# Kernel tuning notes

Hardware: AMD Instinct MI355X
Metric: run time of the kernel (lower is better)

## Reference

```python
import jax, jax.numpy as jnp
import numpy as np

SEQ, B = 1, 250  # fixed by module's hardcoded reshapes


def gru_scan(x_seq, h0, Wih, Whh, bih, bhh):
    """PyTorch-convention GRU. x_seq: (S,B,In), h0: (B,H). Returns (y (S,B,H), hN (B,H))."""
    H = h0.shape[-1]

    def step(h, x_t):
        gi = x_t @ Wih.T + bih            # (B, 3H)
        gh = h @ Whh.T + bhh              # (B, 3H)
        i_r, i_z, i_n = jnp.split(gi, 3, axis=-1)
        h_r, h_z, h_n = jnp.split(gh, 3, axis=-1)
        r = jax.nn.sigmoid(i_r + h_r)
        z = jax.nn.sigmoid(i_z + h_z)
        n = jnp.tanh(i_n + r * h_n)
        h_new = (1.0 - z) * n + z * h
        return h_new, h_new

    hN, y = jax.lax.scan(step, h0, x_seq)
    return y, hN


def setup_inputs() -> dict:
    key = jax.random.key(0)
    ks = jax.random.split(key, 13)
    s = 0.1
    return {
        "x": jax.random.normal(ks[0], (250,), dtype=jnp.float32),
        "enc_Wih": jax.random.normal(ks[1], (12, 1), dtype=jnp.float32) * s,
        "enc_Whh": jax.random.normal(ks[2], (12, 4), dtype=jnp.float32) * s,
        "enc_bih": jax.random.normal(ks[3], (12,), dtype=jnp.float32) * s,
        "enc_bhh": jax.random.normal(ks[4], (12,), dtype=jnp.float32) * s,
        "fc1_W": jax.random.normal(ks[5], (512, 1000), dtype=jnp.float32) * 0.03,
        "fc1_b": jax.random.normal(ks[6], (512,), dtype=jnp.float32) * s,
        "fc2_W": jax.random.normal(ks[7], (250, 512), dtype=jnp.float32) * 0.04,
        "fc2_b": jax.random.normal(ks[8], (250,), dtype=jnp.float32) * s,
        "dec_Wih": jax.random.normal(ks[9], (3, 4), dtype=jnp.float32) * s,
        "dec_Whh": jax.random.normal(ks[10], (3, 1), dtype=jnp.float32) * s,
        "dec_bih": jax.random.normal(ks[11], (3,), dtype=jnp.float32) * s,
        "dec_bhh": jax.random.normal(ks[12], (3,), dtype=jnp.float32) * s,
    }


def reference(x, enc_Wih, enc_Whh, enc_bih, enc_bhh, fc1_W, fc1_b, fc2_W, fc2_b,
              dec_Wih, dec_Whh, dec_bih, dec_bhh):
    # Encoder
    x_seq = x.reshape(SEQ, B, 1)                      # (1, 250, 1)
    h0_enc = jnp.zeros((B, 4), dtype=x.dtype)
    y, hN = gru_scan(x_seq, h0_enc, enc_Wih, enc_Whh, enc_bih, enc_bhh)  # y (1,250,4)
    stacked = hN.reshape(1, 1000)
    hn_hid = jax.nn.relu(stacked @ fc1_W.T + fc1_b)   # (1, 512)
    hn = hn_hid @ fc2_W.T + fc2_b                     # (1, 250)
    # Decoder
    h0_dec = hn.reshape(B, 1)                         # (250, 1)
    yrec, _ = gru_scan(y, h0_dec, dec_Wih, dec_Whh, dec_bih, dec_bhh)    # (1, 250, 1)
    return yrec.reshape(250, 1)
```

## Files before the change

kernel.cpp:

```cpp
#include <hip/hip_runtime.h>
#include <math.h>

__device__ __forceinline__ float sigm(float x) { return 1.0f / (1.0f + __expf(-x)); }

__device__ __forceinline__ void enc_step(float xb, const float* __restrict__ Wih,
                                         const float* __restrict__ bih,
                                         const float* __restrict__ bhh, float h[4]) {
#pragma unroll
    for (int j = 0; j < 4; ++j) {
        float ir = fmaf(xb, Wih[j],     bih[j])     + bhh[j];
        float iz = fmaf(xb, Wih[4 + j], bih[4 + j]) + bhh[4 + j];
        float in_ = fmaf(xb, Wih[8 + j], bih[8 + j]);
        float hn  = bhh[8 + j];
        float r = sigm(ir);
        float z = sigm(iz);
        float n = tanhf(fmaf(r, hn, in_));
        h[j] = (1.0f - z) * n;
    }
}

__global__ __launch_bounds__(256) void fused(const float* __restrict__ x,
                                             const float* __restrict__ eWih,
                                             const float* __restrict__ ebih,
                                             const float* __restrict__ ebhh,
                                             const float* __restrict__ fc1W,
                                             const float* __restrict__ fc1b,
                                             const float* __restrict__ fc2W,
                                             const float* __restrict__ fc2b,
                                             const float* __restrict__ dWih,
                                             const float* __restrict__ dWhh,
                                             const float* __restrict__ dbih,
                                             const float* __restrict__ dbhh,
                                             float* __restrict__ partial,
                                             unsigned* __restrict__ counter,
                                             float* __restrict__ out) {
    __shared__ float stacked[1000];
    __shared__ float hid4[4];
    __shared__ unsigned oldc;
    const int t = threadIdx.x;
    const int wave = t >> 6, lane = t & 63;
    const int b = blockIdx.x;

    if (t < 250) {
        float h[4];
        enc_step(x[t], eWih, ebih, ebhh, h);
        ((float4*)stacked)[t] = make_float4(h[0], h[1], h[2], h[3]);
    }
    __syncthreads();

    const int j = b * 4 + wave;
    const float4* w4 = (const float4*)(fc1W + j * 1000);
    const float4* s4 = (const float4*)stacked;
    float s = 0.0f;
#pragma unroll
    for (int q = 0; q < 4; ++q) {
        const int k = lane + q * 64;
        if (k < 250) {
            float4 a = s4[k], w = w4[k];
            s = fmaf(a.x, w.x, s);
            s = fmaf(a.y, w.y, s);
            s = fmaf(a.z, w.z, s);
            s = fmaf(a.w, w.w, s);
        }
    }
#pragma unroll
    for (int m = 32; m >= 1; m >>= 1) s += __shfl_xor(s, m, 64);
    if (lane == 0) hid4[wave] = fmaxf(s + fc1b[j], 0.0f);
    __syncthreads();

    const float h0 = hid4[0], h1 = hid4[1], h2 = hid4[2], h3 = hid4[3];
    if (t < 250) {
        const float4 w2 = *(const float4*)(fc2W + t * 512 + b * 4);
        float p = fmaf(w2.x, h0, fmaf(w2.y, h1, fmaf(w2.z, h2, w2.w * h3)));
        __hip_atomic_store(&partial[b * 256 + t], p,
                           __ATOMIC_RELAXED, __HIP_MEMORY_SCOPE_AGENT);
    }
    asm volatile("s_waitcnt vmcnt(0)" ::: "memory");
    __syncthreads();

    if (t == 0)
        oldc = __hip_atomic_fetch_add(counter, 1u,
                                      __ATOMIC_RELAXED, __HIP_MEMORY_SCOPE_AGENT);
    __syncthreads();
    if ((oldc & 127u) != 127u) return;

    if (t < 250) {
        float acc = fc2b[t];
#pragma unroll 32
        for (int bb = 0; bb < 128; ++bb) {
            const float p = __hip_atomic_load(&partial[bb * 256 + t],
                                              __ATOMIC_RELAXED, __HIP_MEMORY_SCOPE_AGENT);
            acc += p;
        }
        const float hn_i = acc;

        const float y0 = stacked[t * 4 + 0], y1 = stacked[t * 4 + 1];
        const float y2 = stacked[t * 4 + 2], y3 = stacked[t * 4 + 3];
        float gi[3];
#pragma unroll
        for (int g = 0; g < 3; ++g) {
            gi[g] = fmaf(y0, dWih[g * 4 + 0],
                    fmaf(y1, dWih[g * 4 + 1],
                    fmaf(y2, dWih[g * 4 + 2],
                    fmaf(y3, dWih[g * 4 + 3], dbih[g]))));
        }
        const float gh0 = fmaf(hn_i, dWhh[0], dbhh[0]);
        const float gh1 = fmaf(hn_i, dWhh[1], dbhh[1]);
        const float gh2 = fmaf(hn_i, dWhh[2], dbhh[2]);
        const float r = sigm(gi[0] + gh0);
        const float z = sigm(gi[1] + gh1);
        const float n = tanhf(fmaf(r, gh2, gi[2]));
        out[t] = fmaf(z, hn_i, (1.0f - z) * n);
    }
}

extern "C" void kernel_launch(void* const* d_in, const int* in_sizes, int n_in,
                              void* d_out, int out_size, void* d_ws, size_t ws_size,
                              hipStream_t stream) {
    const float* x     = (const float*)d_in[0];
    const float* eWih  = (const float*)d_in[1];
    const float* ebih  = (const float*)d_in[3];
    const float* ebhh  = (const float*)d_in[4];
    const float* fc1W  = (const float*)d_in[5];
    const float* fc1b  = (const float*)d_in[6];
    const float* fc2W  = (const float*)d_in[7];
    const float* fc2b  = (const float*)d_in[8];
    const float* dWih  = (const float*)d_in[9];
    const float* dWhh  = (const float*)d_in[10];
    const float* dbih  = (const float*)d_in[11];
    const float* dbhh  = (const float*)d_in[12];
    float* out = (float*)d_out;

    float*    partial = (float*)d_ws;
    unsigned* counter = (unsigned*)((char*)d_ws + 128 * 256 * 4);

    fused<<<128, 256, 0, stream>>>(x, eWih, ebih, ebhh, fc1W, fc1b, fc2W, fc2b,
                                   dWih, dWhh, dbih, dbhh, partial, counter, out);
}
```

Before: 11.94 us.

## Use 32 blocks of 1024 threads and split final reduction across waves

Reshapes the fused kernel from 128 blocks of 256 threads to 32 blocks of 1024 threads, so each block computes 16 fc1 outputs and writes 32 partial rows instead of 128. The last-arriving block now sums the partials with four thread groups of 8 rows each, combines them through shared memory, and then runs the decoder GRU step. The aim is a shorter serial tail reduction and fewer atomic counter arrivals. The cost is less parallelism across CUs for the fc1 weight stream, and each block recomputes the encoder for all 250 elements.

```diff
diff --git a/kernel.cpp b/kernel.cpp
--- a/kernel.cpp
+++ b/kernel.cpp
@@ -19,23 +19,24 @@
     }
 }
 
-__global__ __launch_bounds__(256) void fused(const float* __restrict__ x,
-                                             const float* __restrict__ eWih,
-                                             const float* __restrict__ ebih,
-                                             const float* __restrict__ ebhh,
-                                             const float* __restrict__ fc1W,
-                                             const float* __restrict__ fc1b,
-                                             const float* __restrict__ fc2W,
-                                             const float* __restrict__ fc2b,
-                                             const float* __restrict__ dWih,
-                                             const float* __restrict__ dWhh,
-                                             const float* __restrict__ dbih,
-                                             const float* __restrict__ dbhh,
-                                             float* __restrict__ partial,
-                                             unsigned* __restrict__ counter,
-                                             float* __restrict__ out) {
+__global__ __launch_bounds__(1024) void fused(const float* __restrict__ x,
+                                              const float* __restrict__ eWih,
+                                              const float* __restrict__ ebih,
+                                              const float* __restrict__ ebhh,
+                                              const float* __restrict__ fc1W,
+                                              const float* __restrict__ fc1b,
+                                              const float* __restrict__ fc2W,
+                                              const float* __restrict__ fc2b,
+                                              const float* __restrict__ dWih,
+                                              const float* __restrict__ dWhh,
+                                              const float* __restrict__ dbih,
+                                              const float* __restrict__ dbhh,
+                                              float* __restrict__ partial,
+                                              unsigned* __restrict__ counter,
+                                              float* __restrict__ out) {
     __shared__ float stacked[1000];
-    __shared__ float hid4[4];
+    __shared__ float hid16[16];
+    __shared__ float psum[1024];
     __shared__ unsigned oldc;
     const int t = threadIdx.x;
     const int wave = t >> 6, lane = t & 63;
@@ -48,7 +49,7 @@
     }
     __syncthreads();
 
-    const int j = b * 4 + wave;
+    const int j = b * 16 + wave;
     const float4* w4 = (const float4*)(fc1W + j * 1000);
     const float4* s4 = (const float4*)stacked;
     float s = 0.0f;
@@ -65,13 +66,20 @@
     }
 #pragma unroll
     for (int m = 32; m >= 1; m >>= 1) s += __shfl_xor(s, m, 64);
-    if (lane == 0) hid4[wave] = fmaxf(s + fc1b[j], 0.0f);
+    if (lane == 0) hid16[wave] = fmaxf(s + fc1b[j], 0.0f);
     __syncthreads();
 
-    const float h0 = hid4[0], h1 = hid4[1], h2 = hid4[2], h3 = hid4[3];
     if (t < 250) {
-        const float4 w2 = *(const float4*)(fc2W + t * 512 + b * 4);
-        float p = fmaf(w2.x, h0, fmaf(w2.y, h1, fmaf(w2.z, h2, w2.w * h3)));
+        const float4* w2 = (const float4*)(fc2W + t * 512 + b * 16);
+        float p = 0.0f;
+#pragma unroll
+        for (int o = 0; o < 4; ++o) {
+            const float4 w = w2[o];
+            p = fmaf(w.x, hid16[o * 4 + 0],
+                fmaf(w.y, hid16[o * 4 + 1],
+                fmaf(w.z, hid16[o * 4 + 2],
+                fmaf(w.w, hid16[o * 4 + 3], p))));
+        }
         __hip_atomic_store(&partial[b * 256 + t], p,
                            __ATOMIC_RELAXED, __HIP_MEMORY_SCOPE_AGENT);
     }
@@ -82,20 +90,25 @@
         oldc = __hip_atomic_fetch_add(counter, 1u,
                                       __ATOMIC_RELAXED, __HIP_MEMORY_SCOPE_AGENT);
     __syncthreads();
-    if ((oldc & 127u) != 127u) return;
+    if ((oldc & 31u) != 31u) return;
 
-    if (t < 250) {
-        float acc = fc2b[t];
-#pragma unroll 32
-        for (int bb = 0; bb < 128; ++bb) {
-            const float p = __hip_atomic_load(&partial[bb * 256 + t],
-                                              __ATOMIC_RELAXED, __HIP_MEMORY_SCOPE_AGENT);
-            acc += p;
+    const int qq = t >> 8;
+    const int i  = t & 255;
+    if (i < 250) {
+        float a = 0.0f;
+#pragma unroll
+        for (int bb = qq * 8; bb < qq * 8 + 8; ++bb) {
+            a += __hip_atomic_load(&partial[bb * 256 + i],
+                                   __ATOMIC_RELAXED, __HIP_MEMORY_SCOPE_AGENT);
         }
-        const float hn_i = acc;
-
-        const float y0 = stacked[t * 4 + 0], y1 = stacked[t * 4 + 1];
-        const float y2 = stacked[t * 4 + 2], y3 = stacked[t * 4 + 3];
+        psum[qq * 256 + i] = a;
+    }
+    __syncthreads();
+    if (qq == 0 && i < 250) {
+        const float hn_i = fc2b[i] + ((psum[i] + psum[256 + i])
+                                    + (psum[512 + i] + psum[768 + i]));
+        const float y0 = stacked[i * 4 + 0], y1 = stacked[i * 4 + 1];
+        const float y2 = stacked[i * 4 + 2], y3 = stacked[i * 4 + 3];
         float gi[3];
 #pragma unroll
         for (int g = 0; g < 3; ++g) {
@@ -110,7 +123,7 @@
         const float r = sigm(gi[0] + gh0);
         const float z = sigm(gi[1] + gh1);
         const float n = tanhf(fmaf(r, gh2, gi[2]));
-        out[t] = fmaf(z, hn_i, (1.0f - z) * n);
+        out[i] = fmaf(z, hn_i, (1.0f - z) * n);
     }
 }
 
@@ -132,8 +145,8 @@
     float* out = (float*)d_out;
 
     float*    partial = (float*)d_ws;
-    unsigned* counter = (unsigned*)((char*)d_ws + 128 * 256 * 4);
+    unsigned* counter = (unsigned*)((char*)d_ws + 32 * 256 * 4);
 
-    fused<<<128, 256, 0, stream>>>(x, eWih, ebih, ebhh, fc1W, fc1b, fc2W, fc2b,
+    fused<<<32, 1024, 0, stream>>>(x, eWih, ebih, ebhh, fc1W, fc1b, fc2W, fc2b,
                                    dWih, dWhh, dbih, dbhh, partial, counter, out);
 }
```

Result: faster. 10.05 us (-15.8%).
